# Kernel tuning notes

Measured on AMD Instinct MI355X. Metric: run time of the kernel, lower is better.

The kernel has to match this reference:

```python
import jax, jax.numpy as jnp
import numpy as np

B, S, D, H = 2, 2048, 1024, 16
HD = D // H  # head_dim = 64
ROPE_BASE = 10000.0
NEG = -1e9


def rope_cos_sin(seq_len, head_dim, dtype):
    inv_freq = 1.0 / (ROPE_BASE ** (jnp.arange(0, head_dim, 2, dtype=jnp.float32) / head_dim))
    t = jnp.arange(seq_len, dtype=jnp.float32)
    freqs = jnp.outer(t, inv_freq)              # [S, HD/2]
    emb = jnp.concatenate([freqs, freqs], axis=-1)  # [S, HD]
    return jnp.cos(emb).astype(dtype), jnp.sin(emb).astype(dtype)


def rotate_half(x):
    half = x.shape[-1] // 2
    return jnp.concatenate([-x[..., half:], x[..., :half]], axis=-1)


def setup_inputs() -> dict:
    key = jax.random.key(0)
    ks = jax.random.split(key, 9)
    s = 0.02
    x = jax.random.normal(ks[0], (B, S, D), dtype=jnp.float32)
    # additive causal mask: 0 on/below diagonal, -1e9 above
    mask = jnp.where(jnp.tril(jnp.ones((S, S), dtype=bool)), 0.0, NEG).astype(jnp.float32)
    params = {
        'Wq': jax.random.normal(ks[1], (D, D), jnp.float32) * s,
        'bq': jnp.zeros((D,), jnp.float32),
        'Wk': jax.random.normal(ks[2], (D, D), jnp.float32) * s,
        'bk': jnp.zeros((D,), jnp.float32),
        'Wv': jax.random.normal(ks[3], (D, D), jnp.float32) * s,
        'bv': jnp.zeros((D,), jnp.float32),
        'Wo': jax.random.normal(ks[4], (D, D), jnp.float32) * s,
        'bo': jnp.zeros((D,), jnp.float32),
    }
    return {'x': x, 'mask': mask, **params}


def reference(x, mask, Wq, bq, Wk, bk, Wv, bv, Wo, bo):
    Bv, Sv, Dv = x.shape
    q = (x @ Wq + bq).reshape(Bv, Sv, H, HD).transpose(0, 2, 1, 3)  # [B,H,S,HD]
    k = (x @ Wk + bk).reshape(Bv, Sv, H, HD).transpose(0, 2, 1, 3)
    v = (x @ Wv + bv).reshape(Bv, Sv, H, HD).transpose(0, 2, 1, 3)
    cos, sin = rope_cos_sin(Sv, HD, x.dtype)      # [S, HD]
    cos = cos[None, None]                          # [1,1,S,HD]
    sin = sin[None, None]
    q = q * cos + rotate_half(q) * sin
    k = k * cos + rotate_half(k) * sin
    scale = jnp.asarray(np.sqrt(HD), x.dtype)
    scores = jnp.einsum('bhqd,bhkd->bhqk', q, k) / scale  # [B,H,S,S]
    scores = scores + mask[None, None]
    attn = jax.nn.softmax(scores, axis=-1)
    out = jnp.einsum('bhqk,bhkd->bhqd', attn, v)   # [B,H,S,HD]
    out = out.transpose(0, 2, 1, 3).reshape(Bv, Sv, Dv)
    return out @ Wo + bo
```

## Files before the change

### kernel.cpp

```cpp
#include <hip/hip_runtime.h>
#include <hip/hip_bf16.h>
#include <cstdint>

typedef __bf16 bf16;
typedef __bf16 bf16x4 __attribute__((ext_vector_type(4)));
typedef __bf16 bf16x8 __attribute__((ext_vector_type(8)));
typedef float f32x4 __attribute__((ext_vector_type(4)));

#define DEV __device__ __forceinline__

DEV void gl_lds16(const void* g, void* l) {
    __builtin_amdgcn_global_load_lds(
        (__attribute__((address_space(1))) void*)(uintptr_t)g,
        (__attribute__((address_space(3))) void*)(uint32_t)(uintptr_t)l,
        16, 0, 0);
}

DEV f32x4 mfma16(bf16x8 a, bf16x8 b, f32x4 c) {
    return __builtin_amdgcn_mfma_f32_16x16x32_bf16(a, b, c, 0, 0, 0);
}

__global__ __launch_bounds__(256) void prep_k(
    const float* __restrict__ x, bf16* __restrict__ xb,
    const float* __restrict__ w0, const float* __restrict__ w1,
    const float* __restrict__ w2, const float* __restrict__ w3,
    bf16* __restrict__ WT, float* __restrict__ cosT, float* __restrict__ sinT) {
    __shared__ float t[32][33];
    const int blk = (int)blockIdx.x;
    const int tid = threadIdx.x;
    if (blk < 4096) {
        const int i = blk * 256 + tid;
        const float4 v = ((const float4*)x)[i];
        bf16x4 o = {(bf16)v.x, (bf16)v.y, (bf16)v.z, (bf16)v.w};
        *(bf16x4*)(xb + (size_t)i * 4) = o;
    } else if (blk < 8192) {
        const int j = blk - 4096;
        const int z = j >> 10, jy = (j >> 5) & 31, jx = j & 31;
        const float* W = z == 0 ? w0 : z == 1 ? w1 : z == 2 ? w2 : w3;
        bf16* dst = WT + (size_t)z * 1024 * 1024;
        const int tx = tid & 31, ty = tid >> 5;
        const int kb = jx * 32, nb = jy * 32;
#pragma unroll
        for (int i = 0; i < 4; ++i)
            t[ty + i * 8][tx] = W[(size_t)(kb + ty + i * 8) * 1024 + nb + tx];
        __syncthreads();
#pragma unroll
        for (int i = 0; i < 4; ++i)
            dst[(size_t)(nb + ty + i * 8) * 1024 + kb + tx] = (bf16)t[tx][ty + i * 8];
    } else {
        const int tt = (blk - 8192) * 256 + tid;
        const int s = tt >> 6, i = tt & 31;
        const float inv = expf(-(float)i * (9.210340371976184f / 32.0f));
        const float ang = (float)s * inv;
        cosT[tt] = cosf(ang);
        sinT[tt] = sinf(ang);
    }
}

template <int MODE>
__global__ __launch_bounds__(256) void gemm_k(
    const bf16* __restrict__ A, const bf16* __restrict__ BT,
    const float* __restrict__ bias0, const float* __restrict__ bias1,
    const float* __restrict__ bias2,
    bf16* __restrict__ outQ, bf16* __restrict__ outK, bf16* __restrict__ outV,
    const float* __restrict__ cosT, const float* __restrict__ sinT,
    float* __restrict__ outF) {
    extern __shared__ char smem[];
    const int tid = threadIdx.x;
    const int lane = tid & 63;
    const int wv = tid >> 6;
    const int wm = wv >> 1, wn = wv & 1;
    const int bm = blockIdx.x, bn = blockIdx.y;
    const int q = lane & 15, g = lane >> 4;

    const bf16* Ab = A + (size_t)bm * 128 * 1024;
    const bf16* Bb = BT + (size_t)bn * 128 * 1024;
    const int r0 = tid >> 2, c0 = (tid & 3) * 8;

    auto stage = [&](int b, int kb) {
        char* base = smem + b * 16384;
        gl_lds16(Ab + (size_t)r0 * 1024 + kb + c0, base + tid * 16);
        gl_lds16(Ab + (size_t)(r0 + 64) * 1024 + kb + c0, base + 4096 + tid * 16);
        gl_lds16(Bb + (size_t)r0 * 1024 + kb + c0, base + 8192 + tid * 16);
        gl_lds16(Bb + (size_t)(r0 + 64) * 1024 + kb + c0, base + 12288 + tid * 16);
    };

    f32x4 acc[4][4] = {};

    stage(0, 0);
    stage(1, 32);
    asm volatile("s_waitcnt vmcnt(4)" ::: "memory");
    __builtin_amdgcn_s_barrier();

    for (int kt = 0; kt < 32; ++kt) {
        if (kt + 2 < 32) stage((kt + 2) % 3, (kt + 2) * 32);
        const bf16* As = (const bf16*)(smem + (kt % 3) * 16384);
        const bf16* Bs = As + 128 * 32;
        bf16x8 af[4], bfr[4];
#pragma unroll
        for (int mi = 0; mi < 4; ++mi)
            af[mi] = *(const bf16x8*)(As + (wm * 64 + mi * 16 + q) * 32 + g * 8);
#pragma unroll
        for (int ni = 0; ni < 4; ++ni)
            bfr[ni] = *(const bf16x8*)(Bs + (wn * 64 + ni * 16 + q) * 32 + g * 8);
#pragma unroll
        for (int mi = 0; mi < 4; ++mi)
#pragma unroll
            for (int ni = 0; ni < 4; ++ni)
                acc[mi][ni] = mfma16(af[mi], bfr[ni], acc[mi][ni]);
        if (kt + 2 < 32) asm volatile("s_waitcnt vmcnt(4)" ::: "memory");
        else             asm volatile("s_waitcnt vmcnt(0)" ::: "memory");
        __builtin_amdgcn_s_barrier();
    }

    const int n0 = bn * 128 + wn * 64;
    if constexpr (MODE == 0) {
        const int seg = n0 >> 10;
        const int nloc = n0 & 1023;
        const int h = nloc >> 6;
        const float* bias = seg == 0 ? bias0 : (seg == 1 ? bias1 : bias2);
        const float qsc = (seg == 0) ? 0.125f : 1.0f;
        float bvv[4];
#pragma unroll
        for (int ni = 0; ni < 4; ++ni) bvv[ni] = bias[nloc + ni * 16 + q];
        if (seg < 2) {
            bf16* dst = seg == 0 ? outQ : outK;
#pragma unroll
            for (int mi = 0; mi < 4; ++mi) {
#pragma unroll
                for (int r = 0; r < 4; ++r) {
                    const int m = bm * 128 + wm * 64 + mi * 16 + g * 4 + r;
                    const int s = m & 2047, bb = m >> 11;
                    const size_t rowb = ((size_t)((bb << 4) | h) * 2048 + s) * 64;
#pragma unroll
                    for (int ni = 0; ni < 4; ++ni) {
                        const int hd = ni * 16 + q;
                        const float c = cosT[s * 64 + hd], sn = sinT[s * 64 + hd];
                        const float v0 = acc[mi][ni][r] + bvv[ni];
                        const float v1 = acc[mi][ni ^ 2][r] + bvv[ni ^ 2];
                        dst[rowb + hd] = (bf16)((v0 * c + (ni < 2 ? -v1 : v1) * sn) * qsc);
                    }
                }
            }
        } else {
            bf16* Tw = (bf16*)smem + wv * (64 * 72);
#pragma unroll
            for (int mi = 0; mi < 4; ++mi)
#pragma unroll
                for (int ni = 0; ni < 4; ++ni)
#pragma unroll
                    for (int r = 0; r < 4; ++r)
                        Tw[(ni * 16 + q) * 72 + mi * 16 + g * 4 + r] =
                            (bf16)(acc[mi][ni][r] + bvv[ni]);
            const int mstart = bm * 128 + wm * 64;
            const int s0 = mstart & 2047, bb = mstart >> 11;
            bf16* vbase = outV + (size_t)((bb << 4) | h) * (64 * 2048);
#pragma unroll
            for (int i = 0; i < 8; ++i) {
                const int row = i * 8 + (lane >> 3);
                const int col = (lane & 7) * 8;
                bf16x8 vvv = *(const bf16x8*)(Tw + row * 72 + col);
                *(bf16x8*)(vbase + (size_t)row * 2048 + s0 + col) = vvv;
            }
        }
    } else {
        float bvv[4];
#pragma unroll
        for (int ni = 0; ni < 4; ++ni) bvv[ni] = bias0[n0 + ni * 16 + q];
#pragma unroll
        for (int mi = 0; mi < 4; ++mi)
#pragma unroll
            for (int r = 0; r < 4; ++r) {
                const int m = bm * 128 + wm * 64 + mi * 16 + g * 4 + r;
#pragma unroll
                for (int ni = 0; ni < 4; ++ni)
                    outF[(size_t)m * 1024 + n0 + ni * 16 + q] = acc[mi][ni][r] + bvv[ni];
            }
    }
}

__global__ __launch_bounds__(512, 2) void attn_k(const bf16* __restrict__ Qr,
                                                 const bf16* __restrict__ Kr,
                                                 const bf16* __restrict__ Vt,
                                                 bf16* __restrict__ AO) {
    const int gid = (int)blockIdx.x;
    const int xcd = gid & 7;
    const int bh = xcd + 8 * ((gid >> 3) & 3);
    const int idx = gid >> 5;
    const int p = idx >> 1;
    const int h = 1 - (idx & 1);
    const int tid = threadIdx.x;
    const int lane = tid & 63, wv = tid >> 6;
    const int q = lane & 15, g = lane >> 4;
    const int qt_w = (wv >> 2) ? p : (15 - p);
    const int q0w = qt_w * 128 + h * 64 + (wv & 3) * 16;
    const int nt = 31 - 2 * p + h;
    const size_t hb = (size_t)bh * (2048 * 64);
    extern __shared__ char smem[];
    bf16* P = (bf16*)(smem + 49152 + wv * 2304);

    const bf16* Kg = Kr + hb;
    const bf16* Vg = Vt + hb;
    const int swz = (q & 7) << 4;

    auto stage = [&](int b, int kb) {
        char* base = smem + b * 16384;
        {
            const int X = tid * 16;
            const int row = X >> 7;
            const int cbg = (X & 127) ^ ((row & 7) << 4);
            gl_lds16(Kg + (size_t)(kb + row) * 64 + (cbg >> 1), base + X);
        }
        {
            const int X = tid * 16;
            const int row = X >> 7;
            const int cbg = (X & 127) ^ ((row & 7) << 4);
            gl_lds16(Vg + (size_t)row * 2048 + kb + (cbg >> 1), base + 8192 + X);
        }
    };

    bf16x8 qf[2];
    {
        const bf16* qp = Qr + hb + (size_t)(q0w + q) * 64 + g * 8;
        qf[0] = *(const bf16x8*)(qp);
        qf[1] = *(const bf16x8*)(qp + 32);
    }
    f32x4 o[4] = {};
    float l_run = 0.0f;
    const f32x4 z4 = {0.f, 0.f, 0.f, 0.f};
    const int rmax = q0w + 15;

    stage(0, 0);
    stage(1, 64);
    asm volatile("s_waitcnt vmcnt(2)" ::: "memory");
    __builtin_amdgcn_s_barrier();

    for (int kt = 0; kt < nt; ++kt) {
        const int kb = kt * 64;
        if (kt + 2 < nt) stage((kt + 2) % 3, kb + 128);
        if (kb <= rmax) {
            char* Kl = smem + (kt % 3) * 16384;
            char* Vl = Kl + 8192;
            f32x4 st[4];
            __builtin_amdgcn_s_setprio(1);
#pragma unroll
            for (int f = 0; f < 4; ++f) {
                const int row = f * 16 + q;
                const bf16x8 k0 = *(const bf16x8*)(Kl + row * 128 + ((g * 16) ^ swz));
                const bf16x8 k1 = *(const bf16x8*)(Kl + row * 128 + ((64 + g * 16) ^ swz));
                f32x4 t0 = mfma16(k0, qf[0], z4);
                st[f] = mfma16(k1, qf[1], t0);
            }
            __builtin_amdgcn_s_setprio(0);
            bf16x8 vf[4][2];
#pragma unroll
            for (int nf = 0; nf < 4; ++nf) {
                const int row = nf * 16 + q;
                vf[nf][0] = *(const bf16x8*)(Vl + row * 128 + ((g * 16) ^ swz));
                vf[nf][1] = *(const bf16x8*)(Vl + row * 128 + ((64 + g * 16) ^ swz));
            }
            const bool maskT = (kb + 63 > q0w);
            float tsum = 0.f;
#pragma unroll
            for (int f = 0; f < 4; ++f)
#pragma unroll
                for (int r = 0; r < 4; ++r) {
                    float sv = st[f][r];
                    if (maskT && (kb + f * 16 + g * 4 + r > q0w + q)) sv = -3.0e38f;
                    const float pv = __expf(fminf(sv, 20.0f));
                    st[f][r] = pv;
                    tsum += pv;
                }
            l_run += tsum;
#pragma unroll
            for (int f = 0; f < 4; ++f) {
                bf16x4 pv = {(bf16)st[f][0], (bf16)st[f][1],
                             (bf16)st[f][2], (bf16)st[f][3]};
                *(bf16x4*)&P[q * 72 + f * 16 + g * 4] = pv;
            }
            __builtin_amdgcn_s_setprio(1);
#pragma unroll
            for (int t = 0; t < 2; ++t) {
                const bf16x8 pa = *(const bf16x8*)&P[q * 72 + t * 32 + g * 8];
#pragma unroll
                for (int nf = 0; nf < 4; ++nf)
                    o[nf] = mfma16(pa, vf[nf][t], o[nf]);
            }
            __builtin_amdgcn_s_setprio(0);
        }
        if (kt + 2 < nt) asm volatile("s_waitcnt vmcnt(2)" ::: "memory");
        else             asm volatile("s_waitcnt vmcnt(0)" ::: "memory");
        __builtin_amdgcn_s_barrier();
    }

    l_run += __shfl_xor(l_run, 16);
    l_run += __shfl_xor(l_run, 32);
    float li[4];
#pragma unroll
    for (int r = 0; r < 4; ++r) li[r] = 1.0f / __shfl(l_run, g * 4 + r);
    const int b_ = bh >> 4, h_ = bh & 15;
#pragma unroll
    for (int nf = 0; nf < 4; ++nf)
#pragma unroll
        for (int r = 0; r < 4; ++r) {
            const int qg = q0w + g * 4 + r;
            AO[(size_t)(b_ * 2048 + qg) * 1024 + h_ * 64 + nf * 16 + q] =
                (bf16)(o[nf][r] * li[r]);
        }
}


extern "C" void kernel_launch(void* const* d_in, const int* in_sizes, int n_in,
                              void* d_out, int out_size, void* d_ws, size_t ws_size,
                              hipStream_t stream) {
    const float* x  = (const float*)d_in[0];
    const float* Wq = (const float*)d_in[2];
    const float* bq = (const float*)d_in[3];
    const float* Wk = (const float*)d_in[4];
    const float* bk = (const float*)d_in[5];
    const float* Wv = (const float*)d_in[6];
    const float* bv = (const float*)d_in[7];
    const float* Wo = (const float*)d_in[8];
    const float* bo = (const float*)d_in[9];
    float* out = (float*)d_out;
    char* ws = (char*)d_ws;
    const size_t MB_ = 1024 * 1024;
    bf16* xb    = (bf16*)(ws);
    bf16* WT    = (bf16*)(ws + 8 * MB_);
    bf16* Qrp   = (bf16*)(ws + 16 * MB_);
    bf16* Krp   = (bf16*)(ws + 24 * MB_);
    bf16* Vt    = (bf16*)(ws + 32 * MB_);
    bf16* AO    = (bf16*)(ws + 40 * MB_);
    float* cosT = (float*)(ws + 48 * MB_);
    float* sinT = (float*)(ws + 48 * MB_ + 512 * 1024);

    prep_k<<<8704, 256, 0, stream>>>(x, xb, Wq, Wk, Wv, Wo, WT, cosT, sinT);
    gemm_k<0><<<dim3(32, 24), 256, 49152, stream>>>(xb, WT, bq, bk, bv, Qrp, Krp, Vt,
                                                    cosT, sinT, nullptr);
    attn_k<<<dim3(512, 1), 512, 67584, stream>>>(Qrp, Krp, Vt, AO);
    gemm_k<1><<<dim3(32, 8), 256, 49152, stream>>>(AO, WT + (size_t)3072 * 1024, bo,
                                                   nullptr, nullptr, nullptr, nullptr,
                                                   nullptr, nullptr, nullptr, out);
}
```

Measured before the change: 103.6 us.

## Use 256x256 tiled QKV GEMM with swizzled LDS and XCD-aware block mapping

Replaces the 128x128 QKV projection GEMM with a 256x256 tile kernel using 512 threads, 128KB of double-buffered LDS with an XOR swizzle, K-steps of 64, and s_setprio around the MFMA bursts. The 192 blocks are remapped so tiles sharing A/B rows land on the same XCD for L2 reuse. The RoPE/bias epilogue is kept but extended to 8 M-subtiles per wave. The output GEMM is split into its own non-templated kernel. Larger tiles raise arithmetic intensity but give only 192 blocks on a 256-CU part, so some CUs sit idle; the high LDS use also limits occupancy.

```diff
diff --git a/kernel.cpp b/kernel.cpp
--- a/kernel.cpp
+++ b/kernel.cpp
@@ -57,14 +57,138 @@
     }
 }
 
-template <int MODE>
-__global__ __launch_bounds__(256) void gemm_k(
+__global__ __launch_bounds__(512, 2) void gemm256_k(
     const bf16* __restrict__ A, const bf16* __restrict__ BT,
-    const float* __restrict__ bias0, const float* __restrict__ bias1,
-    const float* __restrict__ bias2,
+    const float* __restrict__ bq, const float* __restrict__ bk,
+    const float* __restrict__ bv,
     bf16* __restrict__ outQ, bf16* __restrict__ outK, bf16* __restrict__ outV,
-    const float* __restrict__ cosT, const float* __restrict__ sinT,
-    float* __restrict__ outF) {
+    const float* __restrict__ cosT, const float* __restrict__ sinT) {
+    extern __shared__ char smem[];
+    const int tid = threadIdx.x;
+    const int lane = tid & 63, wv = tid >> 6;
+    const int wm2 = wv >> 2, wn2 = wv & 3;
+    const int q = lane & 15, g = lane >> 4;
+
+    const int gid = (int)blockIdx.x;
+    const int xcd = gid & 7, idx = gid >> 3;
+    const int bm = (xcd & 3) * 4 + (idx & 3);
+    const int bn = (xcd >> 2) * 6 + (idx >> 2);
+
+    const bf16* Ab = A + (size_t)bm * 256 * 1024;
+    const bf16* Bb = BT + (size_t)bn * 256 * 1024;
+
+    auto stageQ = [&](int b, int kb, int qq) {
+        char* sect = smem + b * 65536 + (qq >> 1) * 32768;
+        const bf16* src = (qq >> 1) ? Bb : Ab;
+        const int half = qq & 1;
+#pragma unroll
+        for (int i = 0; i < 2; ++i) {
+            const int Xs = half * 16384 + i * 8192 + tid * 16;
+            const int row = Xs >> 7;
+            const int cb = (Xs & 127) ^ ((row & 7) << 4);
+            gl_lds16(src + (size_t)row * 1024 + kb + (cb >> 1), sect + Xs);
+        }
+    };
+
+    f32x4 acc[8][4] = {};
+
+#pragma unroll
+    for (int qq = 0; qq < 4; ++qq) stageQ(0, 0, qq);
+
+    for (int t = 0; t < 16; ++t) {
+        asm volatile("s_waitcnt vmcnt(0)" ::: "memory");
+        __builtin_amdgcn_s_barrier();
+        const char* cbuf = smem + (t & 1) * 65536;
+        bf16x8 bfr[4];
+#pragma unroll
+        for (int p = 0; p < 4; ++p) {
+            const int ks = p >> 1, mih = p & 1;
+            if (t + 1 < 16) stageQ((t + 1) & 1, (t + 1) * 64, p);
+            if (mih == 0) {
+#pragma unroll
+                for (int ni = 0; ni < 4; ++ni) {
+                    const int row = wn2 * 64 + ni * 16 + q;
+                    bfr[ni] = *(const bf16x8*)(cbuf + 32768 + row * 128 +
+                                               ((ks * 64 + g * 16) ^ ((q & 7) << 4)));
+                }
+            }
+            bf16x8 af[4];
+#pragma unroll
+            for (int j = 0; j < 4; ++j) {
+                const int row = wm2 * 128 + (mih * 4 + j) * 16 + q;
+                af[j] = *(const bf16x8*)(cbuf + row * 128 +
+                                         ((ks * 64 + g * 16) ^ ((q & 7) << 4)));
+            }
+            __builtin_amdgcn_s_barrier();
+            __builtin_amdgcn_s_setprio(1);
+#pragma unroll
+            for (int j = 0; j < 4; ++j)
+#pragma unroll
+                for (int ni = 0; ni < 4; ++ni)
+                    acc[mih * 4 + j][ni] = mfma16(af[j], bfr[ni], acc[mih * 4 + j][ni]);
+            __builtin_amdgcn_s_setprio(0);
+            __builtin_amdgcn_s_barrier();
+        }
+    }
+
+    const int n0 = bn * 256 + wn2 * 64;
+    const int seg = n0 >> 10;
+    const int nloc = n0 & 1023;
+    const int h = nloc >> 6;
+    const float* bias = seg == 0 ? bq : (seg == 1 ? bk : bv);
+    const float qsc = (seg == 0) ? 0.125f : 1.0f;
+    float bvv[4];
+#pragma unroll
+    for (int ni = 0; ni < 4; ++ni) bvv[ni] = bias[nloc + ni * 16 + q];
+
+    if (seg < 2) {
+        bf16* dst = seg == 0 ? outQ : outK;
+#pragma unroll
+        for (int mi = 0; mi < 8; ++mi) {
+#pragma unroll
+            for (int r = 0; r < 4; ++r) {
+                const int m = bm * 256 + wm2 * 128 + mi * 16 + g * 4 + r;
+                const int s = m & 2047, bb = m >> 11;
+                const size_t rowb = ((size_t)((bb << 4) | h) * 2048 + s) * 64;
+#pragma unroll
+                for (int ni = 0; ni < 4; ++ni) {
+                    const int hd = ni * 16 + q;
+                    const float c = cosT[s * 64 + hd], sn = sinT[s * 64 + hd];
+                    const float v0 = acc[mi][ni][r] + bvv[ni];
+                    const float v1 = acc[mi][ni ^ 2][r] + bvv[ni ^ 2];
+                    dst[rowb + hd] = (bf16)((v0 * c + (ni < 2 ? -v1 : v1) * sn) * qsc);
+                }
+            }
+        }
+    } else {
+        bf16* Tw = (bf16*)smem + wv * (64 * 72);
+        const int bb = (bm * 256) >> 11;
+        bf16* vbase = outV + (size_t)((bb << 4) | h) * (64 * 2048);
+#pragma unroll
+        for (int sh = 0; sh < 2; ++sh) {
+#pragma unroll
+            for (int mi2 = 0; mi2 < 4; ++mi2)
+#pragma unroll
+                for (int ni = 0; ni < 4; ++ni)
+#pragma unroll
+                    for (int r = 0; r < 4; ++r)
+                        Tw[(ni * 16 + q) * 72 + mi2 * 16 + g * 4 + r] =
+                            (bf16)(acc[sh * 4 + mi2][ni][r] + bvv[ni]);
+            const int s0 = ((bm * 256) & 2047) + wm2 * 128 + sh * 64;
+#pragma unroll
+            for (int i = 0; i < 8; ++i) {
+                const int row = i * 8 + (lane >> 3);
+                const int col = (lane & 7) * 8;
+                bf16x8 vvv = *(const bf16x8*)(Tw + row * 72 + col);
+                *(bf16x8*)(vbase + (size_t)row * 2048 + s0 + col) = vvv;
+            }
+        }
+    }
+}
+
+__global__ __launch_bounds__(256) void gemmo_k(
+    const bf16* __restrict__ A, const bf16* __restrict__ BT,
+    const float* __restrict__ bias0, float* __restrict__ outF) {
     extern __shared__ char smem[];
     const int tid = threadIdx.x;
     const int lane = tid & 63;
@@ -114,69 +238,18 @@
     }
 
     const int n0 = bn * 128 + wn * 64;
-    if constexpr (MODE == 0) {
-        const int seg = n0 >> 10;
-        const int nloc = n0 & 1023;
-        const int h = nloc >> 6;
-        const float* bias = seg == 0 ? bias0 : (seg == 1 ? bias1 : bias2);
-        const float qsc = (seg == 0) ? 0.125f : 1.0f;
-        float bvv[4];
-#pragma unroll
-        for (int ni = 0; ni < 4; ++ni) bvv[ni] = bias[nloc + ni * 16 + q];
-        if (seg < 2) {
-            bf16* dst = seg == 0 ? outQ : outK;
-#pragma unroll
-            for (int mi = 0; mi < 4; ++mi) {
-#pragma unroll
-                for (int r = 0; r < 4; ++r) {
-                    const int m = bm * 128 + wm * 64 + mi * 16 + g * 4 + r;
-                    const int s = m & 2047, bb = m >> 11;
-                    const size_t rowb = ((size_t)((bb << 4) | h) * 2048 + s) * 64;
-#pragma unroll
-                    for (int ni = 0; ni < 4; ++ni) {
-                        const int hd = ni * 16 + q;
-                        const float c = cosT[s * 64 + hd], sn = sinT[s * 64 + hd];
-                        const float v0 = acc[mi][ni][r] + bvv[ni];
-                        const float v1 = acc[mi][ni ^ 2][r] + bvv[ni ^ 2];
-                        dst[rowb + hd] = (bf16)((v0 * c + (ni < 2 ? -v1 : v1) * sn) * qsc);
-                    }
-                }
-            }
-        } else {
-            bf16* Tw = (bf16*)smem + wv * (64 * 72);
-#pragma unroll
-            for (int mi = 0; mi < 4; ++mi)
-#pragma unroll
-                for (int ni = 0; ni < 4; ++ni)
-#pragma unroll
-                    for (int r = 0; r < 4; ++r)
-                        Tw[(ni * 16 + q) * 72 + mi * 16 + g * 4 + r] =
-                            (bf16)(acc[mi][ni][r] + bvv[ni]);
-            const int mstart = bm * 128 + wm * 64;
-            const int s0 = mstart & 2047, bb = mstart >> 11;
-            bf16* vbase = outV + (size_t)((bb << 4) | h) * (64 * 2048);
-#pragma unroll
-            for (int i = 0; i < 8; ++i) {
-                const int row = i * 8 + (lane >> 3);
-                const int col = (lane & 7) * 8;
-                bf16x8 vvv = *(const bf16x8*)(Tw + row * 72 + col);
-                *(bf16x8*)(vbase + (size_t)row * 2048 + s0 + col) = vvv;
-            }
-        }
-    } else {
-        float bvv[4];
-#pragma unroll
-        for (int ni = 0; ni < 4; ++ni) bvv[ni] = bias0[n0 + ni * 16 + q];
-#pragma unroll
-        for (int mi = 0; mi < 4; ++mi)
-#pragma unroll
-            for (int r = 0; r < 4; ++r) {
-                const int m = bm * 128 + wm * 64 + mi * 16 + g * 4 + r;
-#pragma unroll
-                for (int ni = 0; ni < 4; ++ni)
-                    outF[(size_t)m * 1024 + n0 + ni * 16 + q] = acc[mi][ni][r] + bvv[ni];
-            }
-    }
+    float bvv[4];
+#pragma unroll
+    for (int ni = 0; ni < 4; ++ni) bvv[ni] = bias0[n0 + ni * 16 + q];
+#pragma unroll
+    for (int mi = 0; mi < 4; ++mi)
+#pragma unroll
+        for (int r = 0; r < 4; ++r) {
+            const int m = bm * 128 + wm * 64 + mi * 16 + g * 4 + r;
+#pragma unroll
+            for (int ni = 0; ni < 4; ++ni)
+                outF[(size_t)m * 1024 + n0 + ni * 16 + q] = acc[mi][ni][r] + bvv[ni];
+        }
 }
 
 __global__ __launch_bounds__(512, 2) void attn_k(const bf16* __restrict__ Qr,
@@ -334,11 +407,12 @@
     float* cosT = (float*)(ws + 48 * MB_);
     float* sinT = (float*)(ws + 48 * MB_ + 512 * 1024);
 
+    hipFuncSetAttribute((const void*)gemm256_k,
+                        hipFuncAttributeMaxDynamicSharedMemorySize, 131072);
+
     prep_k<<<8704, 256, 0, stream>>>(x, xb, Wq, Wk, Wv, Wo, WT, cosT, sinT);
-    gemm_k<0><<<dim3(32, 24), 256, 49152, stream>>>(xb, WT, bq, bk, bv, Qrp, Krp, Vt,
-                                                    cosT, sinT, nullptr);
+    gemm256_k<<<dim3(192), 512, 131072, stream>>>(xb, WT, bq, bk, bv,
+                                                  Qrp, Krp, Vt, cosT, sinT);
     attn_k<<<dim3(512, 1), 512, 67584, stream>>>(Qrp, Krp, Vt, AO);
-    gemm_k<1><<<dim3(32, 8), 256, 49152, stream>>>(AO, WT + (size_t)3072 * 1024, bo,
-                                                   nullptr, nullptr, nullptr, nullptr,
-                                                   nullptr, nullptr, nullptr, out);
-}
+    gemmo_k<<<dim3(32, 8), 256, 49152, stream>>>(AO, WT + (size_t)3072 * 1024, bo, out);
+}
```

Measured after the change: 102.4 us. About the same (-1.2%).
